# Kernel optimization log

Hardware: AMD Instinct MI355X
Metric: run time of the kernel (lower is better)

Reference implementation:

```python
import jax, jax.numpy as jnp
import numpy as np

CHANNELS = 128
M_MODES = 64
B = 128
N = 4096


def setup_inputs() -> dict:
    key = jax.random.key(0)
    k1, k2, k3 = jax.random.split(key, 3)
    h = jax.random.normal(k1, (B * N, CHANNELS), dtype=jnp.float32)
    U = jax.random.normal(k2, (B, N, M_MODES), dtype=jnp.float32)
    W = jax.random.normal(k3, (M_MODES, CHANNELS, CHANNELS), dtype=jnp.float32) * 0.02
    ptr = jnp.arange(B + 1, dtype=jnp.int64) * N  # equal-size segments
    return {"h": h, "U": U, "W": W, "ptr": ptr}


def reference(h, U, W, ptr):
    # U: [B, N, m]; h: [B*N, C]; W: [m, C, C]
    b, n, m = U.shape
    hb = h.reshape(b, n, -1)                              # [B, N, C]
    h_hat = jnp.einsum('bnm,bnc->bmc', U, hb)             # U^T h per graph
    out_hat = jnp.einsum('bmc,mco->bmo', h_hat, W)        # per-mode channel mix
    out = jnp.einsum('bnm,bmo->bno', U, out_hat)          # back to node space
    return out.reshape(h.shape)
```

## Files before the change

### kernel.cpp

```cpp
#include <hip/hip_runtime.h>

#define CH 128
#define MM 64
#define BB 128
#define NN 4096
#define KSPLIT 4
#define KCHUNK (NN / KSPLIT)
#define NSTEP (KCHUNK / 32)

typedef __bf16 bf16x8 __attribute__((ext_vector_type(8)));
typedef float  f32x4  __attribute__((ext_vector_type(4)));

__global__ __launch_bounds__(256, 2) void k1_uth(const float* __restrict__ U,
                                                 const float* __restrict__ h,
                                                 float* __restrict__ hhp) {
    const int tid  = threadIdx.x;
    const int lane = tid & 63;
    const int wv   = tid >> 6;
    const int b    = blockIdx.x >> 2;
    const int ks   = blockIdx.x & 3;
    const int k0   = ks * KCHUNK;

    const int l15 = lane & 15;
    const int g   = lane >> 4;
    const int lk  = g * 8;

    const float* Ua = U + ((size_t)b * NN + k0 + lk) * MM + 2 * l15;
    const float* ha = h + ((size_t)b * NN + k0 + lk) * CH + wv * 32 + 2 * l15;

    float2 ar[2][2][8];
    float2 br[2][8];

    auto load_step = [&](int buf, int step) {
        const float* ua = Ua + (size_t)step * 32 * MM;
        const float* hb = ha + (size_t)step * 32 * CH;
        #pragma unroll
        for (int j = 0; j < 8; ++j) {
            ar[buf][0][j] = *(const float2*)(ua + j * MM);
            ar[buf][1][j] = *(const float2*)(ua + j * MM + 32);
        }
        #pragma unroll
        for (int j = 0; j < 8; ++j)
            br[buf][j] = *(const float2*)(hb + j * CH);
    };

    f32x4 acc[4][2];
    #pragma unroll
    for (int t = 0; t < 4; ++t)
        #pragma unroll
        for (int ci = 0; ci < 2; ++ci)
            acc[t][ci] = (f32x4){0.f, 0.f, 0.f, 0.f};

    auto compute = [&](int buf) {
        bf16x8 af[4], bfr[2];
        #pragma unroll
        for (int j = 0; j < 8; ++j) {
            af[0][j]  = (__bf16)ar[buf][0][j].x;
            af[1][j]  = (__bf16)ar[buf][0][j].y;
            af[2][j]  = (__bf16)ar[buf][1][j].x;
            af[3][j]  = (__bf16)ar[buf][1][j].y;
            bfr[0][j] = (__bf16)br[buf][j].x;
            bfr[1][j] = (__bf16)br[buf][j].y;
        }
        #pragma unroll
        for (int t = 0; t < 4; ++t)
            #pragma unroll
            for (int ci = 0; ci < 2; ++ci)
                acc[t][ci] = __builtin_amdgcn_mfma_f32_16x16x32_bf16(
                    af[t], bfr[ci], acc[t][ci], 0, 0, 0);
    };

    load_step(0, 0);
    #pragma unroll 2
    for (int t = 0; t < NSTEP - 1; ++t) {
        load_step((t + 1) & 1, t + 1);
        compute(t & 1);
    }
    compute((NSTEP - 1) & 1);

    float* dst = hhp + (size_t)(b * KSPLIT + ks) * MM * CH + wv * 32 + 2 * l15;
    #pragma unroll
    for (int t = 0; t < 4; ++t)
        #pragma unroll
        for (int r = 0; r < 4; ++r) {
            const int m = (t >> 1) * 32 + 2 * (g * 4 + r) + (t & 1);
            *(float2*)(dst + (size_t)m * CH) =
                make_float2(acc[t][0][r], acc[t][1][r]);
        }
}

__global__ __launch_bounds__(256) void k2_mix(const float* __restrict__ hhp,
                                              const float* __restrict__ W,
                                              __bf16* __restrict__ ohf) {
    __shared__ float hs[16][CH];
    const int tid  = threadIdx.x;
    const int o    = tid & 127;
    const int half = tid >> 7;
    const int m    = blockIdx.x;
    const int b0   = blockIdx.y * 16;

    #pragma unroll
    for (int i = 0; i < 8; ++i) {
        const int b = b0 + half * 8 + i;
        const float* src = hhp + ((size_t)(b * KSPLIT) * MM + m) * CH + o;
        float s = 0.f;
        #pragma unroll
        for (int ksi = 0; ksi < KSPLIT; ++ksi)
            s += src[(size_t)ksi * MM * CH];
        hs[half * 8 + i][o] = s;
    }
    __syncthreads();

    float acc[8];
    #pragma unroll
    for (int i = 0; i < 8; ++i) acc[i] = 0.f;

    const float* Wm = W + (size_t)m * CH * CH;
    for (int c = 0; c < CH; ++c) {
        const float w = Wm[c * CH + o];
        #pragma unroll
        for (int i = 0; i < 8; ++i) acc[i] += hs[half * 8 + i][c] * w;
    }

    const int mt      = m >> 5;
    const int m5      = m & 31;
    const int lane_hi = m5 >> 3;
    const int j       = m5 & 7;
    const int ot      = o >> 4;
    const int lane    = lane_hi * 16 + (o & 15);
    const size_t eidx = ((size_t)(mt * 8 + ot) * 64 + lane) * 8 + j;

    #pragma unroll
    for (int i = 0; i < 8; ++i) {
        const int b = b0 + half * 8 + i;
        ohf[(size_t)b * 8192 + eidx] = (__bf16)acc[i];
    }
}

__global__ __launch_bounds__(256) void k3_back(const float* __restrict__ U,
                                               const __bf16* __restrict__ ohf,
                                               float* __restrict__ out) {
    const int tid  = threadIdx.x;
    const int lane = tid & 63;
    const int wv   = tid >> 6;
    const int n0   = blockIdx.x * 64;
    const int b    = blockIdx.y;

    const bf16x8* ohfb = (const bf16x8*)(ohf + (size_t)b * 8192);
    bf16x8 bf[2][8];
    #pragma unroll
    for (int mt = 0; mt < 2; ++mt)
        #pragma unroll
        for (int ot = 0; ot < 8; ++ot)
            bf[mt][ot] = ohfb[(mt * 8 + ot) * 64 + lane];

    const float* arow = U + ((size_t)b * NN + n0 + wv * 16 + (lane & 15)) * MM
                          + ((lane >> 4) << 3);
    bf16x8 af[2];
    #pragma unroll
    for (int mt = 0; mt < 2; ++mt) {
        float4 a0 = *(const float4*)(arow + mt * 32);
        float4 a1 = *(const float4*)(arow + mt * 32 + 4);
        af[mt][0] = (__bf16)a0.x; af[mt][1] = (__bf16)a0.y;
        af[mt][2] = (__bf16)a0.z; af[mt][3] = (__bf16)a0.w;
        af[mt][4] = (__bf16)a1.x; af[mt][5] = (__bf16)a1.y;
        af[mt][6] = (__bf16)a1.z; af[mt][7] = (__bf16)a1.w;
    }

    f32x4 acc[8];
    #pragma unroll
    for (int ot = 0; ot < 8; ++ot) acc[ot] = (f32x4){0.f, 0.f, 0.f, 0.f};

    #pragma unroll
    for (int ot = 0; ot < 8; ++ot) {
        acc[ot] = __builtin_amdgcn_mfma_f32_16x16x32_bf16(af[0], bf[0][ot], acc[ot], 0, 0, 0);
        acc[ot] = __builtin_amdgcn_mfma_f32_16x16x32_bf16(af[1], bf[1][ot], acc[ot], 0, 0, 0);
    }

    float* dst = out + ((size_t)b * NN + n0 + wv * 16 + (lane >> 4) * 4) * CH + (lane & 15);
    #pragma unroll
    for (int ot = 0; ot < 8; ++ot)
        #pragma unroll
        for (int r = 0; r < 4; ++r)
            dst[(size_t)r * CH + ot * 16] = acc[ot][r];
}

extern "C" void kernel_launch(void* const* d_in, const int* in_sizes, int n_in,
                              void* d_out, int out_size, void* d_ws, size_t ws_size,
                              hipStream_t stream) {
    const float* h = (const float*)d_in[0];
    const float* U = (const float*)d_in[1];
    const float* W = (const float*)d_in[2];
    float* out = (float*)d_out;

    float*  hhp = (float*)d_out;
    __bf16* ohf = (__bf16*)d_ws;

    k1_uth<<<BB * KSPLIT, 256, 0, stream>>>(U, h, hhp);
    k2_mix<<<dim3(MM, BB / 16), 256, 0, stream>>>(hhp, W, ohf);
    k3_back<<<dim3(NN / 64, BB), 256, 0, stream>>>(U, ohf, out);
}
```

Measured before the change: 219.4 us.

## Stage k1 operand tiles through LDS with async global_load_lds triple buffering

Replaces the per-lane register double-buffered global loads in the U^T h kernel with direct global-to-LDS asynchronous copies into a three-stage shared-memory ring. Threads cooperatively load contiguous 16-byte chunks, then read fragments back from LDS for bf16 conversion and MFMA. The aim is to get fully coalesced wide loads and deeper prefetch while freeing registers. In exchange it adds LDS traffic, two barriers per step, and LDS use that may limit occupancy, with manual vmcnt waits that must match the issued load count.

```diff
diff --git a/kernel.cpp b/kernel.cpp
--- a/kernel.cpp
+++ b/kernel.cpp
@@ -6,14 +6,28 @@
 #define NN 4096
 #define KSPLIT 4
 #define KCHUNK (NN / KSPLIT)
-#define NSTEP (KCHUNK / 32)
+#define KSTEP 32
+#define NSTEP (KCHUNK / KSTEP)
+
+#define UBUF (KSTEP * MM)
+#define HBUF (KSTEP * CH)
+#define BUF  (UBUF + HBUF)
 
 typedef __bf16 bf16x8 __attribute__((ext_vector_type(8)));
 typedef float  f32x4  __attribute__((ext_vector_type(4)));
+
+#define AS1(p) ((const __attribute__((address_space(1))) void*)(p))
+#define AS3(p) ((__attribute__((address_space(3))) void*)(p))
+
+__device__ __forceinline__ void gl_lds16(const float* g, float* l) {
+    __builtin_amdgcn_global_load_lds(AS1(g), AS3(l), 16, 0, 0);
+}
 
 __global__ __launch_bounds__(256, 2) void k1_uth(const float* __restrict__ U,
                                                  const float* __restrict__ h,
                                                  float* __restrict__ hhp) {
+    __shared__ float lds[3 * BUF];
+
     const int tid  = threadIdx.x;
     const int lane = tid & 63;
     const int wv   = tid >> 6;
@@ -25,23 +39,19 @@
     const int g   = lane >> 4;
     const int lk  = g * 8;
 
-    const float* Ua = U + ((size_t)b * NN + k0 + lk) * MM + 2 * l15;
-    const float* ha = h + ((size_t)b * NN + k0 + lk) * CH + wv * 32 + 2 * l15;
-
-    float2 ar[2][2][8];
-    float2 br[2][8];
-
-    auto load_step = [&](int buf, int step) {
-        const float* ua = Ua + (size_t)step * 32 * MM;
-        const float* hb = ha + (size_t)step * 32 * CH;
-        #pragma unroll
-        for (int j = 0; j < 8; ++j) {
-            ar[buf][0][j] = *(const float2*)(ua + j * MM);
-            ar[buf][1][j] = *(const float2*)(ua + j * MM + 32);
-        }
-        #pragma unroll
-        for (int j = 0; j < 8; ++j)
-            br[buf][j] = *(const float2*)(hb + j * CH);
+    const float* Ub = U + ((size_t)b * NN + k0) * MM;
+    const float* hb = h + ((size_t)b * NN + k0) * CH;
+
+    auto stage = [&](int s, int t) {
+        float* dst = &lds[s * BUF];
+        const float* us = Ub + (size_t)t * KSTEP * MM;
+        const float* hs = hb + (size_t)t * KSTEP * CH;
+        gl_lds16(us + tid * 4,        dst + tid * 4);
+        gl_lds16(us + 1024 + tid * 4, dst + 1024 + tid * 4);
+        gl_lds16(hs + tid * 4,        dst + UBUF + tid * 4);
+        gl_lds16(hs + 1024 + tid * 4, dst + UBUF + 1024 + tid * 4);
+        gl_lds16(hs + 2048 + tid * 4, dst + UBUF + 2048 + tid * 4);
+        gl_lds16(hs + 3072 + tid * 4, dst + UBUF + 3072 + tid * 4);
     };
 
     f32x4 acc[4][2];
@@ -51,16 +61,22 @@
         for (int ci = 0; ci < 2; ++ci)
             acc[t][ci] = (f32x4){0.f, 0.f, 0.f, 0.f};
 
-    auto compute = [&](int buf) {
+    auto compute = [&](int s) {
+        const float* P  = &lds[s * BUF];
+        const float* Pa = P + lk * 64 + 2 * l15;
+        const float* Pb = P + UBUF + lk * 128 + wv * 32 + 2 * l15;
         bf16x8 af[4], bfr[2];
         #pragma unroll
         for (int j = 0; j < 8; ++j) {
-            af[0][j]  = (__bf16)ar[buf][0][j].x;
-            af[1][j]  = (__bf16)ar[buf][0][j].y;
-            af[2][j]  = (__bf16)ar[buf][1][j].x;
-            af[3][j]  = (__bf16)ar[buf][1][j].y;
-            bfr[0][j] = (__bf16)br[buf][j].x;
-            bfr[1][j] = (__bf16)br[buf][j].y;
+            float2 a0 = *(const float2*)(Pa + j * 64);
+            float2 a1 = *(const float2*)(Pa + j * 64 + 32);
+            float2 bv = *(const float2*)(Pb + j * 128);
+            af[0][j]  = (__bf16)a0.x;
+            af[1][j]  = (__bf16)a0.y;
+            af[2][j]  = (__bf16)a1.x;
+            af[3][j]  = (__bf16)a1.y;
+            bfr[0][j] = (__bf16)bv.x;
+            bfr[1][j] = (__bf16)bv.y;
         }
         #pragma unroll
         for (int t = 0; t < 4; ++t)
@@ -70,13 +86,23 @@
                     af[t], bfr[ci], acc[t][ci], 0, 0, 0);
     };
 
-    load_step(0, 0);
-    #pragma unroll 2
-    for (int t = 0; t < NSTEP - 1; ++t) {
-        load_step((t + 1) & 1, t + 1);
-        compute(t & 1);
-    }
-    compute((NSTEP - 1) & 1);
+    stage(0, 0);
+    stage(1, 1);
+    #pragma unroll 1
+    for (int t = 0; t < NSTEP; ++t) {
+        if (t + 2 < NSTEP) {
+            stage((t + 2) % 3, t + 2);
+            asm volatile("s_waitcnt vmcnt(12)" ::: "memory");
+        } else if (t + 1 < NSTEP) {
+            asm volatile("s_waitcnt vmcnt(6)" ::: "memory");
+        } else {
+            asm volatile("s_waitcnt vmcnt(0)" ::: "memory");
+        }
+        __builtin_amdgcn_s_barrier();
+        __builtin_amdgcn_sched_barrier(0);
+        compute(t % 3);
+        __builtin_amdgcn_s_barrier();
+    }
 
     float* dst = hhp + (size_t)(b * KSPLIT + ks) * MM * CH + wv * 32 + 2 * l15;
     #pragma unroll
```

Measured after the change: 212.4 us. 3.2% less time.

## Split U^T h over more waves and K-chunks, drop register double-buffering

Applied to the files above, without the earlier changes.

The first kernel now splits the node dimension into 8 chunks instead of 4 and uses 512-thread blocks. Each of its 8 waves covers half the modes and a quarter of the channels, so each wave holds 4 accumulators instead of 8 and far fewer registers. The explicit register double-buffered load pipeline is replaced by a simple non-unrolled loop, with occupancy relied on to hide latency. This raises occupancy and the block count, but the mix kernel must now reduce twice as many partials, and each wave reloads h with less reuse across modes.

```diff
diff --git a/kernel.cpp b/kernel.cpp
--- a/kernel.cpp
+++ b/kernel.cpp
@@ -4,88 +4,74 @@
 #define MM 64
 #define BB 128
 #define NN 4096
-#define KSPLIT 4
+#define KSPLIT 8
 #define KCHUNK (NN / KSPLIT)
 #define NSTEP (KCHUNK / 32)
+#define MMCH (MM * CH)
 
 typedef __bf16 bf16x8 __attribute__((ext_vector_type(8)));
 typedef float  f32x4  __attribute__((ext_vector_type(4)));
 
-__global__ __launch_bounds__(256, 2) void k1_uth(const float* __restrict__ U,
+__global__ __launch_bounds__(512, 6) void k1_uth(const float* __restrict__ U,
                                                  const float* __restrict__ h,
                                                  float* __restrict__ hhp) {
     const int tid  = threadIdx.x;
     const int lane = tid & 63;
     const int wv   = tid >> 6;
-    const int b    = blockIdx.x >> 2;
-    const int ks   = blockIdx.x & 3;
+    const int mh   = wv >> 2;
+    const int cq   = wv & 3;
+    const int b    = blockIdx.x >> 3;
+    const int ks   = blockIdx.x & 7;
     const int k0   = ks * KCHUNK;
 
     const int l15 = lane & 15;
     const int g   = lane >> 4;
     const int lk  = g * 8;
 
-    const float* Ua = U + ((size_t)b * NN + k0 + lk) * MM + 2 * l15;
-    const float* ha = h + ((size_t)b * NN + k0 + lk) * CH + wv * 32 + 2 * l15;
+    const float* Ua = U + ((size_t)b * NN + k0 + lk) * MM + mh * 32 + 2 * l15;
+    const float* ha = h + ((size_t)b * NN + k0 + lk) * CH + cq * 32 + 2 * l15;
 
-    float2 ar[2][2][8];
-    float2 br[2][8];
+    f32x4 acc[2][2];
+    #pragma unroll
+    for (int p = 0; p < 2; ++p)
+        #pragma unroll
+        for (int ci = 0; ci < 2; ++ci)
+            acc[p][ci] = (f32x4){0.f, 0.f, 0.f, 0.f};
 
-    auto load_step = [&](int buf, int step) {
-        const float* ua = Ua + (size_t)step * 32 * MM;
-        const float* hb = ha + (size_t)step * 32 * CH;
+    #pragma unroll 1
+    for (int t = 0; t < NSTEP; ++t) {
+        const float* ua = Ua + (size_t)t * 32 * MM;
+        const float* hb = ha + (size_t)t * 32 * CH;
+        float2 ar[8], br[8];
         #pragma unroll
         for (int j = 0; j < 8; ++j) {
-            ar[buf][0][j] = *(const float2*)(ua + j * MM);
-            ar[buf][1][j] = *(const float2*)(ua + j * MM + 32);
+            ar[j] = *(const float2*)(ua + j * MM);
+            br[j] = *(const float2*)(hb + j * CH);
+        }
+        bf16x8 af[2], bfr[2];
+        #pragma unroll
+        for (int j = 0; j < 8; ++j) {
+            af[0][j]  = (__bf16)ar[j].x;
+            af[1][j]  = (__bf16)ar[j].y;
+            bfr[0][j] = (__bf16)br[j].x;
+            bfr[1][j] = (__bf16)br[j].y;
         }
         #pragma unroll
-        for (int j = 0; j < 8; ++j)
-            br[buf][j] = *(const float2*)(hb + j * CH);
-    };
-
-    f32x4 acc[4][2];
-    #pragma unroll
-    for (int t = 0; t < 4; ++t)
-        #pragma unroll
-        for (int ci = 0; ci < 2; ++ci)
-            acc[t][ci] = (f32x4){0.f, 0.f, 0.f, 0.f};
-
-    auto compute = [&](int buf) {
-        bf16x8 af[4], bfr[2];
-        #pragma unroll
-        for (int j = 0; j < 8; ++j) {
-            af[0][j]  = (__bf16)ar[buf][0][j].x;
-            af[1][j]  = (__bf16)ar[buf][0][j].y;
-            af[2][j]  = (__bf16)ar[buf][1][j].x;
-            af[3][j]  = (__bf16)ar[buf][1][j].y;
-            bfr[0][j] = (__bf16)br[buf][j].x;
-            bfr[1][j] = (__bf16)br[buf][j].y;
-        }
-        #pragma unroll
-        for (int t = 0; t < 4; ++t)
+        for (int p = 0; p < 2; ++p)
             #pragma unroll
             for (int ci = 0; ci < 2; ++ci)
-                acc[t][ci] = __builtin_amdgcn_mfma_f32_16x16x32_bf16(
-                    af[t], bfr[ci], acc[t][ci], 0, 0, 0);
-    };
+                acc[p][ci] = __builtin_amdgcn_mfma_f32_16x16x32_bf16(
+                    af[p], bfr[ci], acc[p][ci], 0, 0, 0);
+    }
 
-    load_step(0, 0);
-    #pragma unroll 2
-    for (int t = 0; t < NSTEP - 1; ++t) {
-        load_step((t + 1) & 1, t + 1);
-        compute(t & 1);
-    }
-    compute((NSTEP - 1) & 1);
-
-    float* dst = hhp + (size_t)(b * KSPLIT + ks) * MM * CH + wv * 32 + 2 * l15;
+    float* dst = hhp + (size_t)(b * KSPLIT + ks) * MMCH + cq * 32 + 2 * l15;
     #pragma unroll
-    for (int t = 0; t < 4; ++t)
+    for (int p = 0; p < 2; ++p)
         #pragma unroll
         for (int r = 0; r < 4; ++r) {
-            const int m = (t >> 1) * 32 + 2 * (g * 4 + r) + (t & 1);
+            const int m = mh * 32 + 2 * (g * 4 + r) + p;
             *(float2*)(dst + (size_t)m * CH) =
-                make_float2(acc[t][0][r], acc[t][1][r]);
+                make_float2(acc[p][0][r], acc[p][1][r]);
         }
 }
 
@@ -106,7 +92,7 @@
         float s = 0.f;
         #pragma unroll
         for (int ksi = 0; ksi < KSPLIT; ++ksi)
-            s += src[(size_t)ksi * MM * CH];
+            s += src[(size_t)ksi * MMCH];
         hs[half * 8 + i][o] = s;
     }
     __syncthreads();
@@ -196,7 +182,7 @@
     float*  hhp = (float*)d_out;
     __bf16* ohf = (__bf16*)d_ws;
 
-    k1_uth<<<BB * KSPLIT, 256, 0, stream>>>(U, h, hhp);
+    k1_uth<<<BB * KSPLIT, 512, 0, stream>>>(U, h, hhp);
     k2_mix<<<dim3(MM, BB / 16), 256, 0, stream>>>(hhp, W, ohf);
     k3_back<<<dim3(NN / 64, BB), 256, 0, stream>>>(U, ohf, out);
 }
```

Result: slower. 231.8 us (+5.6%).
